# Kernel optimization log

Hardware: AMD Instinct MI355X
Metric: run time of the kernel (lower is better)

Reference implementation:

```python
import jax, jax.numpy as jnp
import numpy as np

N = 50000
E = 800000
F = 128
HID = 128
C = 40
GAMMA = 0.1
EPS = 0.1


def gcn(x, theta, src, dst, n):
    # GCNConv (bias=False) with added self-loops and symmetric normalization.
    xw = x @ theta  # [N, d]
    ones = jnp.ones(src.shape[0], dtype=x.dtype)
    deg = jax.ops.segment_sum(ones, dst, num_segments=n) + 1.0  # in-degree incl. self loop
    dinv = jax.lax.rsqrt(deg)
    norm = dinv[src] * dinv[dst]            # [E]
    msg = xw[src] * norm[:, None]           # [E, d]  (dominant memory traffic)
    agg = jax.ops.segment_sum(msg, dst, num_segments=n)
    return agg + xw * (dinv * dinv)[:, None]  # self-loop contribution


def antisym_conv(x, W, bias, theta, src, dst, n):
    # PyG AntiSymmetricConv, num_iters=1, act=tanh, eps=0.1, gamma=0.1
    M = W - W.T - GAMMA * jnp.eye(W.shape[0], dtype=x.dtype)
    h = gcn(x, theta, src, dst, n)
    h = x @ M.T + h + bias
    return x + EPS * jnp.tanh(h)


def setup_inputs() -> dict:
    key = jax.random.key(0)
    ks = jax.random.split(key, 12)
    s = 0.05
    return {
        "x": jax.random.normal(ks[0], (N, F), dtype=jnp.float32),
        "edge_index": jax.random.randint(ks[1], (2, E), 0, N, dtype=jnp.int64)
        if jax.config.jax_enable_x64 else jax.random.randint(ks[1], (2, E), 0, N, dtype=jnp.int32),
        # AntiSymmetricConv 1 (num_features channels)
        "W1": jax.random.normal(ks[2], (F, F), dtype=jnp.float32) * s,
        "b1": jnp.zeros((F,), dtype=jnp.float32),
        "T1": jax.random.normal(ks[3], (F, F), dtype=jnp.float32) * s,
        # AntiSymmetricConv 2 (nhid channels)
        "W2": jax.random.normal(ks[4], (HID, HID), dtype=jnp.float32) * s,
        "b2": jnp.zeros((HID,), dtype=jnp.float32),
        "T2": jax.random.normal(ks[5], (HID, HID), dtype=jnp.float32) * s,
        # Linear layers (torch convention: weight [out, in])
        "lw1": jax.random.normal(ks[6], (HID, F), dtype=jnp.float32) * s,
        "lb1": jnp.zeros((HID,), dtype=jnp.float32),
        "lw2": jax.random.normal(ks[7], (C, HID), dtype=jnp.float32) * s,
        "lb2": jnp.zeros((C,), dtype=jnp.float32),
    }


def reference(x, edge_index, W1, b1, T1, W2, b2, T2, lw1, lb1, lw2, lb2):
    src, dst = edge_index[0], edge_index[1]
    n = x.shape[0]
    # eval mode: dropout is identity
    h = antisym_conv(x, W1, b1, T1, src, dst, n)
    h = jax.nn.relu(h)
    h = h @ lw1.T + lb1
    h = jax.nn.relu(h)
    h = antisym_conv(h, W2, b2, T2, src, dst, n)
    h = jax.nn.relu(h)
    x1 = h
    logits = h @ lw2.T + lb2
    result = jax.nn.log_softmax(logits, axis=-1)
    return (result, x1)
```

## Files before the change

### kernel.cpp

```cpp
#include <hip/hip_runtime.h>
#include <hip/hip_bf16.h>
#include <math.h>

#define GAMMA_ 0.1f
#define EPS_ 0.1f
constexpr int BLK = 256;

typedef __attribute__((ext_vector_type(8))) short short8;
typedef __attribute__((ext_vector_type(4))) float f32x4;
typedef __attribute__((ext_vector_type(2))) float f32x2v;
typedef unsigned char u8;

__device__ inline float bflo(uint u) { union { uint i; float f; } v; v.i = u << 16; return v.f; }
__device__ inline float bfhi(uint u) { union { uint i; float f; } v; v.i = u & 0xffff0000u; return v.f; }
__device__ inline ushort f2bf(float f) {
  union { float f; uint i; } v; v.f = f;
  uint i = v.i;
  return (ushort)((i + 0x7fffu + ((i >> 16) & 1u)) >> 16);
}

#if __has_builtin(__builtin_amdgcn_cvt_pk_f32_fp8) && __has_builtin(__builtin_amdgcn_cvt_pk_fp8_f32)
#define HW_FP8 1
#endif

__device__ inline f32x2v fp8x2_dec_sw(uint raw) {
  f32x2v r;
#pragma unroll
  for (int i = 0; i < 2; ++i) {
    uint b = (raw >> (8 * i)) & 0xffu;
    uint em = b & 0x7fu;
    union { uint u; float f; } o;
    o.u = ((b & 0x80u) << 24) | (0x3C000000u + (em << 20));
    r[i] = (em >= 8u) ? o.f : 0.f;
  }
  return r;
}

__device__ inline f32x2v fp8x2_dec(uint raw) {
#ifdef HW_FP8
  return __builtin_amdgcn_cvt_pk_f32_fp8(raw, false);
#else
  return fp8x2_dec_sw(raw);
#endif
}

__device__ inline uint fp8enc1(float x) {
  union { float f; uint u; } v; v.f = x;
  uint s = (v.u >> 24) & 0x80u;
  uint a = v.u & 0x7fffffffu;
  if (a >= 0x43E00000u) return s | 0x7Eu;
  uint r = a + 0x7FFFFu + ((a >> 20) & 1u);
  if (r < 0x3D800000u) return s;
  return s | (((r - 0x3C000000u) >> 20) & 0x7fu);
}

template<bool HI>
__device__ inline uint fp8x2_enc(float f0, float f1, uint old) {
#ifdef HW_FP8
  return __builtin_amdgcn_cvt_pk_fp8_f32(f0, f1, old, HI);
#else
  uint p = fp8enc1(f0) | (fp8enc1(f1) << 8);
  return HI ? ((old & 0x0000ffffu) | (p << 16)) : ((old & 0xffff0000u) | p);
#endif
}

__global__ void k_count(const int* __restrict__ dst, int* cnt,
                        int* __restrict__ rank, int e) {
  int i = blockIdx.x * BLK + threadIdx.x;
  if (i < e) rank[i] = atomicAdd(&cnt[dst[i]], 1);
}

__global__ void k_scan1(const int* __restrict__ cnt, int* __restrict__ rowp,
                        int* __restrict__ bsum, int n) {
  __shared__ int s[BLK];
  int t = threadIdx.x;
  int i = blockIdx.x * BLK + t;
  int v = (i < n) ? cnt[i] : 0;
  s[t] = v; __syncthreads();
  for (int off = 1; off < BLK; off <<= 1) {
    int u = (t >= off) ? s[t - off] : 0;
    __syncthreads();
    s[t] += u;
    __syncthreads();
  }
  if (i < n) rowp[i] = s[t] - v;
  if (t == BLK - 1) bsum[blockIdx.x] = s[t];
}

__global__ void k_scan2(const int* __restrict__ bsum, int* __restrict__ boff, int nb) {
  __shared__ int s[BLK];
  int t = threadIdx.x;
  int v = (t < nb) ? bsum[t] : 0;
  s[t] = v; __syncthreads();
  for (int off = 1; off < BLK; off <<= 1) {
    int u = (t >= off) ? s[t - off] : 0;
    __syncthreads();
    s[t] += u;
    __syncthreads();
  }
  if (t < nb) boff[t] = s[t] - v;
}

__global__ void k_scan3(const int* __restrict__ boff, int* __restrict__ rowp,
                        const int* __restrict__ cnt, float* __restrict__ dinv,
                        int n, int e) {
  int i = blockIdx.x * BLK + threadIdx.x;
  if (i < n) {
    rowp[i] += boff[blockIdx.x];
    dinv[i] = rsqrtf((float)cnt[i] + 1.0f);
    if (i == 0) rowp[n] = e;
  }
}

__global__ void k_fill(const int* __restrict__ src, const int* __restrict__ dst,
                       const int* __restrict__ rowp, const int* __restrict__ rank,
                       int* __restrict__ csrc, int e) {
  int i = blockIdx.x * BLK + threadIdx.x;
  if (i < e) {
    int d = dst[i];
    csrc[rowp[d] + rank[i]] = src[i];
  }
}

__global__ void k_pack(const float* __restrict__ W1, const float* __restrict__ T1,
                       const float* __restrict__ W2, const float* __restrict__ T2,
                       const float* __restrict__ lw1, const float* __restrict__ lw2,
                       ushort* __restrict__ Bpk1, ushort* __restrict__ Bpk2,
                       ushort* __restrict__ Bpkl, ushort* __restrict__ Bpk2l) {
  int idx = blockIdx.x * BLK + threadIdx.x;
  if (idx < 65536) {
    int which = idx >> 15;
    int e = idx & 32767;
    int k = e >> 8, c = e & 255;
    const float* W = which ? W2 : W1;
    const float* T = which ? T2 : T1;
    float v;
    if (c < 128) {
      v = T[k * 128 + c];
    } else {
      int cc = c - 128;
      v = W[cc * 128 + k] - W[k * 128 + cc] - ((cc == k) ? GAMMA_ : 0.f);
    }
    int kt = k >> 5, q = (k >> 3) & 3, j = k & 7;
    ushort* B = which ? Bpk2 : Bpk1;
    B[(((kt * 4 + q) * 256 + c) << 3) + j] = f2bf(v);
  } else if (idx < 81920) {
    int e = idx - 65536;
    int k = e >> 7, c = e & 127;
    float v = lw1[c * 128 + k];
    int kt = k >> 5, q = (k >> 3) & 3, j = k & 7;
    Bpkl[(((kt * 4 + q) * 128 + c) << 3) + j] = f2bf(v);
  } else {
    int e = idx - 81920;
    if (e < 6144) {
      int k = e / 48, c = e - k * 48;
      float v = (c < 40) ? lw2[c * 128 + k] : 0.f;
      int kt = k >> 5, q = (k >> 3) & 3, j = k & 7;
      Bpk2l[(((kt * 4 + q) * 48 + c) << 3) + j] = f2bf(v);
    }
  }
}

__global__ __launch_bounds__(256) void k_mgemm(
    const float* __restrict__ Av, int nrows,
    const ushort* __restrict__ Bpk, const float* __restrict__ dinv,
    ushort* __restrict__ O1, u8* __restrict__ Oq) {
  __shared__ ushort S[64 * 256];
  const int t = threadIdx.x;
  const int w = t >> 6, l = t & 63;
  const int lr = l & 15, lq = l >> 4;
  const int r0 = blockIdx.x * 64;
#pragma unroll
  for (int it = 0; it < 4; ++it) {
    int chunk = it * 256 + t;
    int row = chunk >> 4, c16 = chunk & 15;
    int gr = min(r0 + row, nrows - 1);
    ushort* p = S + row * 128 + (c16 ^ (row & 7)) * 8;
    const float* A = Av + (size_t)gr * 128 + c16 * 8;
    float4 v0 = *(const float4*)(A);
    float4 v1 = *(const float4*)(A + 4);
    ushort4 o0 = {f2bf(v0.x), f2bf(v0.y), f2bf(v0.z), f2bf(v0.w)};
    ushort4 o1 = {f2bf(v1.x), f2bf(v1.y), f2bf(v1.z), f2bf(v1.w)};
    *(ushort4*)(p) = o0;
    *(ushort4*)(p + 4) = o1;
  }
  __syncthreads();
  f32x4 acc[4][4];
#pragma unroll
  for (int rt = 0; rt < 4; ++rt)
#pragma unroll
    for (int n = 0; n < 4; ++n) acc[rt][n] = f32x4{0.f, 0.f, 0.f, 0.f};
#pragma unroll
  for (int kt = 0; kt < 4; ++kt) {
    short8 af[4];
#pragma unroll
    for (int rt = 0; rt < 4; ++rt) {
      int row = rt * 16 + lr;
      af[rt] = *(const short8*)(S + row * 128 + ((kt * 4 + lq) ^ (row & 7)) * 8);
    }
    const ushort* bbase = Bpk + ((size_t)((kt * 4 + lq) * 256) + w * 64 + lr) * 8;
#pragma unroll
    for (int n = 0; n < 4; ++n) {
      short8 bf = *(const short8*)(bbase + n * 16 * 8);
#pragma unroll
      for (int rt = 0; rt < 4; ++rt)
        acc[rt][n] = __builtin_amdgcn_mfma_f32_16x16x32_bf16(af[rt], bf, acc[rt][n], 0, 0, 0);
    }
  }
  __syncthreads();
#pragma unroll
  for (int rt = 0; rt < 4; ++rt)
#pragma unroll
    for (int n = 0; n < 4; ++n)
#pragma unroll
      for (int r = 0; r < 4; ++r) {
        int row = rt * 16 + lq * 4 + r;
        int col = w * 64 + n * 16 + lr;
        int pcol = col ^ (((row >> 2) & 3) << 3);
        S[row * 256 + pcol] = f2bf(acc[rt][n][r]);
      }
  __syncthreads();
#pragma unroll
  for (int it = 0; it < 4; ++it) {
    int idx = it * 256 + t;
    int row = idx >> 4, c8 = idx & 15;
    if (r0 + row < nrows) {
      int pc = (16 + (c8 ^ ((row >> 2) & 3))) * 8;
      uint4 v = *(const uint4*)(S + row * 256 + pc);
      *(uint4*)(O1 + (size_t)(r0 + row) * 128 + c8 * 8) = v;
    }
  }
#pragma unroll
  for (int it = 0; it < 4; ++it) {
    int idx = it * 256 + t;
    int row = idx >> 4, c8 = idx & 15;
    if (r0 + row < nrows) {
      float di = dinv[r0 + row];
      int pc = (c8 ^ ((row >> 2) & 3)) * 8;
      const uint* p = (const uint*)(S + row * 256 + pc);
      uint u0 = p[0], u1 = p[1], u2 = p[2], u3 = p[3];
      uint lo = fp8x2_enc<false>(bflo(u0) * di, bfhi(u0) * di, 0u);
      lo = fp8x2_enc<true>(bflo(u1) * di, bfhi(u1) * di, lo);
      uint hi = fp8x2_enc<false>(bflo(u2) * di, bfhi(u2) * di, 0u);
      hi = fp8x2_enc<true>(bflo(u3) * di, bfhi(u3) * di, hi);
      uint2 ov = { lo, hi };
      *(uint2*)(Oq + (size_t)(r0 + row) * 128 + c8 * 8) = ov;
    }
  }
}

__device__ inline void gather_node(const u8* __restrict__ xq,
                                   const int* __restrict__ csrc,
                                   int e0, int e1, int l, int node,
                                   float& a0, float& a1) {
  uint su = *(const ushort*)(xq + (size_t)node * 128 + 2 * l);
  f32x2v sf = fp8x2_dec(su);
  a0 = sf[0]; a1 = sf[1];
  int e = e0;
  for (; e + 7 < e1; e += 8) {
    int s[8];
#pragma unroll
    for (int u = 0; u < 8; ++u) s[u] = csrc[e + u];
    uint g[8];
#pragma unroll
    for (int u = 0; u < 8; ++u)
      g[u] = *(const ushort*)(xq + (size_t)s[u] * 128 + 2 * l);
#pragma unroll
    for (int u = 0; u < 8; ++u) {
      f32x2v f = fp8x2_dec(g[u]);
      a0 += f[0]; a1 += f[1];
    }
  }
  if (e + 3 < e1) {
    int s[4];
#pragma unroll
    for (int u = 0; u < 4; ++u) s[u] = csrc[e + u];
    uint g[4];
#pragma unroll
    for (int u = 0; u < 4; ++u)
      g[u] = *(const ushort*)(xq + (size_t)s[u] * 128 + 2 * l);
#pragma unroll
    for (int u = 0; u < 4; ++u) {
      f32x2v f = fp8x2_dec(g[u]);
      a0 += f[0]; a1 += f[1];
    }
    e += 4;
  }
  for (; e < e1; ++e) {
    uint g0 = *(const ushort*)(xq + (size_t)csrc[e] * 128 + 2 * l);
    f32x2v f = fp8x2_dec(g0);
    a0 += f[0]; a1 += f[1];
  }
}

__global__ __launch_bounds__(512) void k_aggl(
    const u8* __restrict__ xq, const ushort* __restrict__ xmb,
    const float* __restrict__ xinf, const float* __restrict__ dinv,
    const int* __restrict__ rowp, const int* __restrict__ csrc,
    const float* __restrict__ bias, const ushort* __restrict__ Bpkl,
    const float* __restrict__ lb1, const ushort* __restrict__ Bpk2,
    ushort* __restrict__ h2b, ushort* __restrict__ xmb2, u8* __restrict__ xq2,
    int n) {
  __shared__ ushort S[32 * 256];
  ushort* Sa = S;
  ushort* Sb = S + 32 * 128;
  const int t = threadIdx.x;
  const int w = t >> 6, l = t & 63;
  const int lr = l & 15, lq = l >> 4;
  const int r0 = blockIdx.x * 32;
#pragma unroll
  for (int i = 0; i < 4; ++i) {
    int lrow = w * 4 + i;
    int node = r0 + lrow;
    float o0 = 0.f, o1 = 0.f;
    if (node < n) {
      float a0, a1;
      gather_node(xq, csrc, rowp[node], rowp[node + 1], l, node, a0, a1);
      float di = dinv[node];
      uint mu = *(const uint*)(xmb + (size_t)node * 128 + 2 * l);
      float h0 = a0 * di + bflo(mu) + bias[2 * l];
      float h1 = a1 * di + bfhi(mu) + bias[2 * l + 1];
      float2 xv = *(const float2*)(xinf + (size_t)node * 128 + 2 * l);
      o0 = fmaxf(xv.x + EPS_ * tanhf(h0), 0.f);
      o1 = fmaxf(xv.y + EPS_ * tanhf(h1), 0.f);
    }
    ushort2 o = { f2bf(o0), f2bf(o1) };
    *(ushort2*)(Sa + lrow * 128 + ((l >> 2) ^ (lrow & 7)) * 8 + (l & 3) * 2) = o;
  }
  __syncthreads();
  f32x4 acc[2];
  acc[0] = f32x4{0.f, 0.f, 0.f, 0.f};
  acc[1] = f32x4{0.f, 0.f, 0.f, 0.f};
#pragma unroll
  for (int kt = 0; kt < 4; ++kt) {
    short8 bf = *(const short8*)(Bpkl + ((size_t)((kt * 4 + lq) * 128) + w * 16 + lr) * 8);
#pragma unroll
    for (int rt = 0; rt < 2; ++rt) {
      int row = rt * 16 + lr;
      short8 af = *(const short8*)(Sa + row * 128 + ((kt * 4 + lq) ^ (row & 7)) * 8);
      acc[rt] = __builtin_amdgcn_mfma_f32_16x16x32_bf16(af, bf, acc[rt], 0, 0, 0);
    }
  }
  {
    int col = w * 16 + lr;
    float bv = lb1[col];
#pragma unroll
    for (int rt = 0; rt < 2; ++rt)
#pragma unroll
      for (int r = 0; r < 4; ++r) {
        int row = rt * 16 + lq * 4 + r;
        ushort hb = f2bf(fmaxf(acc[rt][r] + bv, 0.f));
        if (r0 + row < n)
          h2b[(size_t)(r0 + row) * 128 + col] = hb;
        Sb[row * 128 + ((col >> 3) ^ (row & 7)) * 8 + (col & 7)] = hb;
      }
  }
  __syncthreads();
  f32x4 acc2[2][2];
#pragma unroll
  for (int rt = 0; rt < 2; ++rt)
#pragma unroll
    for (int ct = 0; ct < 2; ++ct) acc2[rt][ct] = f32x4{0.f, 0.f, 0.f, 0.f};
#pragma unroll
  for (int kt = 0; kt < 4; ++kt) {
    short8 af[2];
#pragma unroll
    for (int rt = 0; rt < 2; ++rt) {
      int row = rt * 16 + lr;
      af[rt] = *(const short8*)(Sb + row * 128 + ((kt * 4 + lq) ^ (row & 7)) * 8);
    }
#pragma unroll
    for (int ct = 0; ct < 2; ++ct) {
      const ushort* bb = Bpk2 + ((size_t)((kt * 4 + lq) * 256) + w * 32 + ct * 16 + lr) * 8;
      short8 bf = *(const short8*)bb;
#pragma unroll
      for (int rt = 0; rt < 2; ++rt)
        acc2[rt][ct] = __builtin_amdgcn_mfma_f32_16x16x32_bf16(af[rt], bf, acc2[rt][ct], 0, 0, 0);
    }
  }
  __syncthreads();
#pragma unroll
  for (int rt = 0; rt < 2; ++rt)
#pragma unroll
    for (int ct = 0; ct < 2; ++ct)
#pragma unroll
      for (int r = 0; r < 4; ++r) {
        int row = rt * 16 + lq * 4 + r;
        int col = w * 32 + ct * 16 + lr;
        int pcol = col ^ (((row >> 2) & 3) << 3);
        S[row * 256 + pcol] = f2bf(acc2[rt][ct][r]);
      }
  __syncthreads();
  {
    int row = t >> 4, c8 = t & 15;
    if (r0 + row < n) {
      int pc = (16 + (c8 ^ ((row >> 2) & 3))) * 8;
      uint4 v = *(const uint4*)(S + row * 256 + pc);
      *(uint4*)(xmb2 + (size_t)(r0 + row) * 128 + c8 * 8) = v;
      float di = dinv[r0 + row];
      int pq = (c8 ^ ((row >> 2) & 3)) * 8;
      const uint* p = (const uint*)(S + row * 256 + pq);
      uint u0 = p[0], u1 = p[1], u2 = p[2], u3 = p[3];
      uint lo = fp8x2_enc<false>(bflo(u0) * di, bfhi(u0) * di, 0u);
      lo = fp8x2_enc<true>(bflo(u1) * di, bfhi(u1) * di, lo);
      uint hi = fp8x2_enc<false>(bflo(u2) * di, bfhi(u2) * di, 0u);
      hi = fp8x2_enc<true>(bflo(u3) * di, bfhi(u3) * di, hi);
      uint2 ov = { lo, hi };
      *(uint2*)(xq2 + (size_t)(r0 + row) * 128 + c8 * 8) = ov;
    }
  }
}

__global__ __launch_bounds__(256) void k_aggc(
    const u8* __restrict__ xq, const ushort* __restrict__ xmb,
    const ushort* __restrict__ xinb, const float* __restrict__ dinv,
    const int* __restrict__ rowp, const int* __restrict__ csrc,
    const float* __restrict__ bias, float* __restrict__ outf, int n) {
  int node = blockIdx.x * 4 + (threadIdx.x >> 6);
  if (node >= n) return;
  int l = threadIdx.x & 63;
  float a0, a1;
  gather_node(xq, csrc, rowp[node], rowp[node + 1], l, node, a0, a1);
  float di = dinv[node];
  uint mu = *(const uint*)(xmb + (size_t)node * 128 + 2 * l);
  float h0 = a0 * di + bflo(mu) + bias[2 * l];
  float h1 = a1 * di + bfhi(mu) + bias[2 * l + 1];
  uint xu = *(const uint*)(xinb + (size_t)node * 128 + 2 * l);
  float o0 = fmaxf(bflo(xu) + EPS_ * tanhf(h0), 0.f);
  float o1 = fmaxf(bfhi(xu) + EPS_ * tanhf(h1), 0.f);
  float2 o = { o0, o1 };
  *(float2*)(outf + (size_t)node * 128 + 2 * l) = o;
}

__global__ __launch_bounds__(256) void k_logits2(
    const float* __restrict__ X, const ushort* __restrict__ Bpk,
    const float* __restrict__ lb2, float* __restrict__ out, int n) {
  __shared__ float Ls[64 * 49];
  __shared__ float bl[48];
  const int t = threadIdx.x;
  if (t < 48) bl[t] = (t < 40) ? lb2[t] : 0.f;
  const int w = t >> 6, l = t & 63;
  const int lr = l & 15, lq = l >> 4;
  const int r0 = blockIdx.x * 64;
  const int ar = min(r0 + w * 16 + lr, n - 1);
  const float* Ap = X + (size_t)ar * 128 + lq * 8;
  f32x4 acc[3];
#pragma unroll
  for (int nn = 0; nn < 3; ++nn) acc[nn] = f32x4{0.f, 0.f, 0.f, 0.f};
#pragma unroll
  for (int kt = 0; kt < 4; ++kt) {
    float4 xa = *(const float4*)(Ap + kt * 32);
    float4 xc = *(const float4*)(Ap + kt * 32 + 4);
    short8 af;
    af[0] = (short)f2bf(xa.x); af[1] = (short)f2bf(xa.y);
    af[2] = (short)f2bf(xa.z); af[3] = (short)f2bf(xa.w);
    af[4] = (short)f2bf(xc.x); af[5] = (short)f2bf(xc.y);
    af[6] = (short)f2bf(xc.z); af[7] = (short)f2bf(xc.w);
    const ushort* bbase = Bpk + ((size_t)((kt * 4 + lq) * 48) + lr) * 8;
#pragma unroll
    for (int nn = 0; nn < 3; ++nn) {
      short8 bf = *(const short8*)(bbase + nn * 16 * 8);
      acc[nn] = __builtin_amdgcn_mfma_f32_16x16x32_bf16(af, bf, acc[nn], 0, 0, 0);
    }
  }
  __syncthreads();
#pragma unroll
  for (int nn = 0; nn < 3; ++nn)
#pragma unroll
    for (int r = 0; r < 4; ++r) {
      int row = w * 16 + lq * 4 + r;
      int col = nn * 16 + lr;
      Ls[row * 49 + col] = acc[nn][r] + bl[col];
    }
  __syncthreads();
  int row = t >> 2, q = t & 3;
  if (r0 + row >= n) return;
  const float* Lr = Ls + row * 49 + q * 10;
  float m = -1e30f;
#pragma unroll
  for (int c = 0; c < 10; ++c) m = fmaxf(m, Lr[c]);
  m = fmaxf(m, __shfl_xor(m, 1));
  m = fmaxf(m, __shfl_xor(m, 2));
  float s = 0.f;
#pragma unroll
  for (int c = 0; c < 10; ++c) s += expf(Lr[c] - m);
  s += __shfl_xor(s, 1);
  s += __shfl_xor(s, 2);
  float lse = m + logf(s);
  float* Or = out + (size_t)(r0 + row) * 40 + q * 10;
#pragma unroll
  for (int c = 0; c < 10; ++c) Or[c] = Lr[c] - lse;
}

extern "C" void kernel_launch(void* const* d_in, const int* in_sizes, int n_in,
                              void* d_out, int out_size, void* d_ws, size_t ws_size,
                              hipStream_t stream) {
  const float* x   = (const float*)d_in[0];
  const int*   ei  = (const int*)d_in[1];
  const float* W1  = (const float*)d_in[2];
  const float* b1  = (const float*)d_in[3];
  const float* T1  = (const float*)d_in[4];
  const float* W2  = (const float*)d_in[5];
  const float* b2  = (const float*)d_in[6];
  const float* T2  = (const float*)d_in[7];
  const float* lw1 = (const float*)d_in[8];
  const float* lb1 = (const float*)d_in[9];
  const float* lw2 = (const float*)d_in[10];
  const float* lb2 = (const float*)d_in[11];
  const int N = in_sizes[0] / 128;
  const int E = in_sizes[1] / 2;
  const int* src = ei;
  const int* dst = ei + E;

  float* ws = (float*)d_ws;
  size_t o = 0;
  float* dinv = ws;             o += N;
  int* cnt = (int*)(ws + o);    o += N;
  int* rowp = (int*)(ws + o);   o += (size_t)(N + 4);
  int* csrc = (int*)(ws + o);   o += E;
  int* rank = (int*)(ws + o);   o += E;
  int* bsum = (int*)(ws + o);   o += 256;
  int* boff = (int*)(ws + o);   o += 256;
  o = (o + 3) & ~(size_t)3;
  ushort* us = (ushort*)(ws + o);
  size_t uo = 0;
  ushort* Bpk1 = us + uo;       uo += 32768;
  ushort* Bpk2 = us + uo;       uo += 32768;
  ushort* Bpkl = us + uo;       uo += 16384;
  ushort* Bpk2l = us + uo;      uo += 6144;
  ushort* xmb  = us + uo;       uo += (size_t)N * 128;
  ushort* xmb2 = us + uo;       uo += (size_t)N * 128;
  ushort* h2b  = us + uo;       uo += (size_t)N * 128;
  u8* xq  = (u8*)(us + uo);     uo += (size_t)N * 64;
  u8* xq2 = (u8*)(us + uo);

  float* outp = (float*)d_out;
  float* x1 = outp + (size_t)N * 40;

  int nb_n = (N + BLK - 1) / BLK;
  int nb_e = (E + BLK - 1) / BLK;
  int nb_r = (N + 63) / 64;

  hipMemsetAsync(cnt, 0, (size_t)N * sizeof(int), stream);
  k_count<<<nb_e, BLK, 0, stream>>>(dst, cnt, rank, E);
  k_scan1<<<nb_n, BLK, 0, stream>>>(cnt, rowp, bsum, N);
  k_scan2<<<1, BLK, 0, stream>>>(bsum, boff, nb_n);
  k_scan3<<<nb_n, BLK, 0, stream>>>(boff, rowp, cnt, dinv, N, E);
  k_fill<<<nb_e, BLK, 0, stream>>>(src, dst, rowp, rank, csrc, E);
  k_pack<<<344, BLK, 0, stream>>>(W1, T1, W2, T2, lw1, lw2, Bpk1, Bpk2, Bpkl, Bpk2l);

  k_mgemm<<<nb_r, 256, 0, stream>>>(x, N, Bpk1, dinv, xmb, xq);
  k_aggl<<<(N + 31) / 32, 512, 0, stream>>>(
      xq, xmb, x, dinv, rowp, csrc, b1, Bpkl, lb1, Bpk2, h2b, xmb2, xq2, N);
  k_aggc<<<(N + 3) / 4, 256, 0, stream>>>(
      xq2, xmb2, h2b, dinv, rowp, csrc, b2, x1, N);
  k_logits2<<<(N + 63) / 64, 256, 0, stream>>>(x1, Bpk2l, lb2, outp, N);
}
```

Measured before the change: 174.0 us.

## Fuse second aggregation with logits and log-softmax; vectorize h2b stores

Merges the final aggregation kernel and the logits/log_softmax kernel into one 512-thread kernel. Each wave gathers four nodes, keeps the bf16 results in shared memory and runs the classifier MFMA from there, so x1 is no longer read back from global memory and one launch disappears. It also changes the h2b store in k_aggl from scattered 2-byte writes to coalesced 16-byte rows read out of shared memory. In exchange the fused kernel uses more shared memory, idles two waves during the GEMM, and has a block-wide sync after irregular gathers.

```diff
diff --git a/kernel.cpp b/kernel.cpp
--- a/kernel.cpp
+++ b/kernel.cpp
@@ -350,12 +350,17 @@
       for (int r = 0; r < 4; ++r) {
         int row = rt * 16 + lq * 4 + r;
         ushort hb = f2bf(fmaxf(acc[rt][r] + bv, 0.f));
-        if (r0 + row < n)
-          h2b[(size_t)(r0 + row) * 128 + col] = hb;
         Sb[row * 128 + ((col >> 3) ^ (row & 7)) * 8 + (col & 7)] = hb;
       }
   }
   __syncthreads();
+  {
+    int row = t >> 4, c8 = t & 15;
+    if (r0 + row < n) {
+      uint4 v = *(const uint4*)(Sb + row * 128 + (c8 ^ (row & 7)) * 8);
+      *(uint4*)(h2b + (size_t)(r0 + row) * 128 + c8 * 8) = v;
+    }
+  }
   f32x4 acc2[2][2];
 #pragma unroll
   for (int rt = 0; rt < 2; ++rt)
@@ -411,85 +416,81 @@
   }
 }
 
-__global__ __launch_bounds__(256) void k_aggc(
+__global__ __launch_bounds__(512) void k_aggf(
     const u8* __restrict__ xq, const ushort* __restrict__ xmb,
     const ushort* __restrict__ xinb, const float* __restrict__ dinv,
     const int* __restrict__ rowp, const int* __restrict__ csrc,
-    const float* __restrict__ bias, float* __restrict__ outf, int n) {
-  int node = blockIdx.x * 4 + (threadIdx.x >> 6);
-  if (node >= n) return;
-  int l = threadIdx.x & 63;
-  float a0, a1;
-  gather_node(xq, csrc, rowp[node], rowp[node + 1], l, node, a0, a1);
-  float di = dinv[node];
-  uint mu = *(const uint*)(xmb + (size_t)node * 128 + 2 * l);
-  float h0 = a0 * di + bflo(mu) + bias[2 * l];
-  float h1 = a1 * di + bfhi(mu) + bias[2 * l + 1];
-  uint xu = *(const uint*)(xinb + (size_t)node * 128 + 2 * l);
-  float o0 = fmaxf(bflo(xu) + EPS_ * tanhf(h0), 0.f);
-  float o1 = fmaxf(bfhi(xu) + EPS_ * tanhf(h1), 0.f);
-  float2 o = { o0, o1 };
-  *(float2*)(outf + (size_t)node * 128 + 2 * l) = o;
-}
-
-__global__ __launch_bounds__(256) void k_logits2(
-    const float* __restrict__ X, const ushort* __restrict__ Bpk,
-    const float* __restrict__ lb2, float* __restrict__ out, int n) {
-  __shared__ float Ls[64 * 49];
+    const float* __restrict__ bias, const ushort* __restrict__ Bpk2l,
+    const float* __restrict__ lb2,
+    float* __restrict__ x1, float* __restrict__ outp, int n) {
+  __shared__ ushort Sa[32 * 128];
+  __shared__ float Ls[32 * 49];
   __shared__ float bl[48];
   const int t = threadIdx.x;
   if (t < 48) bl[t] = (t < 40) ? lb2[t] : 0.f;
   const int w = t >> 6, l = t & 63;
   const int lr = l & 15, lq = l >> 4;
-  const int r0 = blockIdx.x * 64;
-  const int ar = min(r0 + w * 16 + lr, n - 1);
-  const float* Ap = X + (size_t)ar * 128 + lq * 8;
-  f32x4 acc[3];
-#pragma unroll
-  for (int nn = 0; nn < 3; ++nn) acc[nn] = f32x4{0.f, 0.f, 0.f, 0.f};
-#pragma unroll
-  for (int kt = 0; kt < 4; ++kt) {
-    float4 xa = *(const float4*)(Ap + kt * 32);
-    float4 xc = *(const float4*)(Ap + kt * 32 + 4);
-    short8 af;
-    af[0] = (short)f2bf(xa.x); af[1] = (short)f2bf(xa.y);
-    af[2] = (short)f2bf(xa.z); af[3] = (short)f2bf(xa.w);
-    af[4] = (short)f2bf(xc.x); af[5] = (short)f2bf(xc.y);
-    af[6] = (short)f2bf(xc.z); af[7] = (short)f2bf(xc.w);
-    const ushort* bbase = Bpk + ((size_t)((kt * 4 + lq) * 48) + lr) * 8;
-#pragma unroll
-    for (int nn = 0; nn < 3; ++nn) {
-      short8 bf = *(const short8*)(bbase + nn * 16 * 8);
-      acc[nn] = __builtin_amdgcn_mfma_f32_16x16x32_bf16(af, bf, acc[nn], 0, 0, 0);
-    }
-  }
-  __syncthreads();
-#pragma unroll
-  for (int nn = 0; nn < 3; ++nn)
+  const int r0 = blockIdx.x * 32;
+#pragma unroll
+  for (int i = 0; i < 4; ++i) {
+    int lrow = w * 4 + i;
+    int node = r0 + lrow;
+    float o0 = 0.f, o1 = 0.f;
+    if (node < n) {
+      float a0, a1;
+      gather_node(xq, csrc, rowp[node], rowp[node + 1], l, node, a0, a1);
+      float di = dinv[node];
+      uint mu = *(const uint*)(xmb + (size_t)node * 128 + 2 * l);
+      float h0 = a0 * di + bflo(mu) + bias[2 * l];
+      float h1 = a1 * di + bfhi(mu) + bias[2 * l + 1];
+      uint xu = *(const uint*)(xinb + (size_t)node * 128 + 2 * l);
+      o0 = fmaxf(bflo(xu) + EPS_ * tanhf(h0), 0.f);
+      o1 = fmaxf(bfhi(xu) + EPS_ * tanhf(h1), 0.f);
+      float2 o = { o0, o1 };
+      *(float2*)(x1 + (size_t)node * 128 + 2 * l) = o;
+    }
+    ushort2 ob = { f2bf(o0), f2bf(o1) };
+    *(ushort2*)(Sa + lrow * 128 + ((l >> 2) ^ (lrow & 7)) * 8 + (l & 3) * 2) = ob;
+  }
+  __syncthreads();
+  if (w < 6) {
+    int rt = w / 3, ct = w % 3;
+    f32x4 acc = f32x4{0.f, 0.f, 0.f, 0.f};
+#pragma unroll
+    for (int kt = 0; kt < 4; ++kt) {
+      int row = rt * 16 + lr;
+      short8 af = *(const short8*)(Sa + row * 128 + ((kt * 4 + lq) ^ (row & 7)) * 8);
+      short8 bf = *(const short8*)(Bpk2l + ((size_t)((kt * 4 + lq) * 48) + ct * 16 + lr) * 8);
+      acc = __builtin_amdgcn_mfma_f32_16x16x32_bf16(af, bf, acc, 0, 0, 0);
+    }
 #pragma unroll
     for (int r = 0; r < 4; ++r) {
-      int row = w * 16 + lq * 4 + r;
-      int col = nn * 16 + lr;
-      Ls[row * 49 + col] = acc[nn][r] + bl[col];
-    }
-  __syncthreads();
-  int row = t >> 2, q = t & 3;
-  if (r0 + row >= n) return;
-  const float* Lr = Ls + row * 49 + q * 10;
-  float m = -1e30f;
-#pragma unroll
-  for (int c = 0; c < 10; ++c) m = fmaxf(m, Lr[c]);
-  m = fmaxf(m, __shfl_xor(m, 1));
-  m = fmaxf(m, __shfl_xor(m, 2));
-  float s = 0.f;
-#pragma unroll
-  for (int c = 0; c < 10; ++c) s += expf(Lr[c] - m);
-  s += __shfl_xor(s, 1);
-  s += __shfl_xor(s, 2);
-  float lse = m + logf(s);
-  float* Or = out + (size_t)(r0 + row) * 40 + q * 10;
-#pragma unroll
-  for (int c = 0; c < 10; ++c) Or[c] = Lr[c] - lse;
+      int row = rt * 16 + lq * 4 + r;
+      int col = ct * 16 + lr;
+      Ls[row * 49 + col] = acc[r] + bl[col];
+    }
+  }
+  __syncthreads();
+  if (t < 128) {
+    int row = t >> 2, q = t & 3;
+    if (r0 + row < n) {
+      const float* Lr = Ls + row * 49 + q * 10;
+      float m = -1e30f;
+#pragma unroll
+      for (int c = 0; c < 10; ++c) m = fmaxf(m, Lr[c]);
+      m = fmaxf(m, __shfl_xor(m, 1));
+      m = fmaxf(m, __shfl_xor(m, 2));
+      float s = 0.f;
+#pragma unroll
+      for (int c = 0; c < 10; ++c) s += expf(Lr[c] - m);
+      s += __shfl_xor(s, 1);
+      s += __shfl_xor(s, 2);
+      float lse = m + logf(s);
+      float* Or = outp + (size_t)(r0 + row) * 40 + q * 10;
+#pragma unroll
+      for (int c = 0; c < 10; ++c) Or[c] = Lr[c] - lse;
+    }
+  }
 }
 
 extern "C" void kernel_launch(void* const* d_in, const int* in_sizes, int n_in,
@@ -552,7 +553,6 @@
   k_mgemm<<<nb_r, 256, 0, stream>>>(x, N, Bpk1, dinv, xmb, xq);
   k_aggl<<<(N + 31) / 32, 512, 0, stream>>>(
       xq, xmb, x, dinv, rowp, csrc, b1, Bpkl, lb1, Bpk2, h2b, xmb2, xq2, N);
-  k_aggc<<<(N + 3) / 4, 256, 0, stream>>>(
-      xq2, xmb2, h2b, dinv, rowp, csrc, b2, x1, N);
-  k_logits2<<<(N + 63) / 64, 256, 0, stream>>>(x1, Bpk2l, lb2, outp, N);
-}
+  k_aggf<<<(N + 31) / 32, 512, 0, stream>>>(
+      xq2, xmb2, h2b, dinv, rowp, csrc, b2, Bpk2l, lb2, x1, outp, N);
+}
```

Result: no change. 171.0 us (-1.8%).
